# Performance work log

Hardware: AMD Instinct MI355X
Metric: run time of the kernel (lower is better)

Reference implementation:

```python
import jax, jax.numpy as jnp
import numpy as np

IMAGE = 800.0
HIGH_THRESH = 0.7   # torchvision RPN fg_iou_thresh
LOW_THRESH = 0.3    # torchvision RPN bg_iou_thresh
BELOW_LOW = -1      # Matcher.BELOW_LOW_THRESHOLD
BETWEEN = -2        # Matcher.BETWEEN_THRESHOLDS


def _make_boxes(key, shape, max_wh):
    # shape = (..., 4) target; build valid xyxy boxes inside the image
    k1, k2 = jax.random.split(key)
    xy = jax.random.uniform(k1, shape[:-1] + (2,)) * (IMAGE - max_wh)
    wh = jax.random.uniform(k2, shape[:-1] + (2,)) * (max_wh - 4.0) + 4.0
    return jnp.concatenate([xy, xy + wh], axis=-1)


def setup_inputs() -> dict:
    key = jax.random.key(0)
    kA, kG, kS, kC = jax.random.split(key, 4)
    B, A, G = 4, 160000, 64
    anchors = _make_boxes(kA, (B, A, 4), 128.0)
    gt_boxes = _make_boxes(kG, (B, G, 4), 200.0)
    # soft score labels in {0, 0.5, 1} style: mostly 1, some <1 (ignored), some 0
    u = jax.random.uniform(kS, (B, G))
    score_labels = jnp.where(u < 0.15, 0.0, jnp.where(u < 0.3, 0.5, 1.0)).astype(jnp.float32)
    confidence_labels = jax.random.randint(kC, (B, G), 0, 2).astype(jnp.int32)
    return {"anchors": anchors, "gt_boxes": gt_boxes,
            "score_labels": score_labels, "confidence_labels": confidence_labels}


def _box_iou(a, b):
    # a: [G,4] gt, b: [A,4] anchors -> [G,A]
    area_a = (a[:, 2] - a[:, 0]) * (a[:, 3] - a[:, 1])          # [G]
    area_b = (b[:, 2] - b[:, 0]) * (b[:, 3] - b[:, 1])          # [A]
    lt = jnp.maximum(a[:, None, :2], b[None, :, :2])            # [G,A,2]
    rb = jnp.minimum(a[:, None, 2:], b[None, :, 2:])            # [G,A,2]
    wh = jnp.clip(rb - lt, 0.0)
    inter = wh[..., 0] * wh[..., 1]                              # [G,A]
    return inter / (area_a[:, None] + area_b[None, :] - inter)


def _matcher(mq):
    # torchvision Matcher with allow_low_quality_matches=True. mq: [G,A]
    matched_vals = mq.max(axis=0)                                # [A]
    matches = mq.argmax(axis=0).astype(jnp.int32)                # [A]
    m = jnp.where(matched_vals < LOW_THRESH, BELOW_LOW,
                  jnp.where(matched_vals < HIGH_THRESH, BETWEEN, matches))
    # restore, for each gt, anchors achieving that gt's max IoU
    highest_per_gt = mq.max(axis=1, keepdims=True)               # [G,1]
    low_quality = (mq == highest_per_gt).any(axis=0)             # [A]
    return jnp.where(low_quality, matches, m)


def _assign_one(anchors, gt, scores, confs):
    mq = _box_iou(gt, anchors)                                   # [G,A]
    midx = _matcher(mq)                                          # [A]
    cl = jnp.clip(midx, 0)
    matched_gt = gt[cl]                                          # [A,4]
    pos = midx >= 0
    labels = pos.astype(jnp.float32)
    labels = jnp.minimum(labels, scores[cl])
    labels = jnp.where(midx == BELOW_LOW, 0.0, labels)
    labels = jnp.where(midx == BETWEEN, -1.0, labels)
    labels = jnp.where((scores[cl] < 1.0) & pos, -1.0, labels)
    labels = jnp.where((confs[cl] == 0) & pos, -1.0, labels)
    return labels, matched_gt


def reference(anchors, gt_boxes, score_labels, confidence_labels):
    labels, matched_gt_boxes = jax.vmap(_assign_one)(anchors, gt_boxes, score_labels, confidence_labels)
    return labels, matched_gt_boxes
```

## Files before the change

kernel.cpp:

```cpp
#include <hip/hip_runtime.h>

constexpr int NB = 4;
constexpr int NA = 160000;
constexpr int NG = 64;

constexpr int P1  = 250;
constexpr int APB = NA / P1;
constexpr int APW = APB / 4;

__device__ __forceinline__ float box_area(float x0, float y0, float x1, float y1) {
#pragma clang fp contract(off)
    return (x1 - x0) * (y1 - y0);
}

__device__ __forceinline__ void inter_denom(float gx0, float gy0, float gx1, float gy1, float garea,
                                            float ax0, float ay0, float ax1, float ay1, float aarea,
                                            float& inter, float& denom) {
#pragma clang fp contract(off)
    float ltx = fmaxf(gx0, ax0);
    float lty = fmaxf(gy0, ay0);
    float rbx = fminf(gx1, ax1);
    float rby = fminf(gy1, ay1);
    float w = fmaxf(rbx - ltx, 0.0f);
    float h = fmaxf(rby - lty, 0.0f);
    inter = w * h;
    float s = garea + aarea;
    denom = s - inter;
}

__device__ __forceinline__ bool frac_gt(float i1, float d1, float i2, float d2) {
#pragma clang fp contract(off)
    float p1 = i1 * d2;
    float p2 = i2 * d1;
    float e1 = fmaf(i1, d2, -p1);
    float e2 = fmaf(i2, d1, -p2);
    return (p1 > p2) || ((p1 == p2) && (e1 > e2));
}

__device__ __forceinline__ float div_rn(float n, float d) {
    float y = __builtin_amdgcn_rcpf(d);
    float e = fmaf(-d, y, 1.0f);
    y = fmaf(e, y, y);
    float q = n * y;
    float r = fmaf(-d, q, n);
    q = fmaf(r, y, q);
    float r2 = fmaf(-d, q, n);
    return fmaf(r2, y, q);
}

__global__ __launch_bounds__(256) void k_part(
        const float* __restrict__ anchors, const float* __restrict__ gts,
        float2* __restrict__ part ) {
    const int b = blockIdx.y;
    const int j = blockIdx.x;
    const int lane = threadIdx.x & 63;
    const int wid = __builtin_amdgcn_readfirstlane(threadIdx.x >> 6);

    const float4* __restrict__ anc =
        reinterpret_cast<const float4*>(anchors) + (size_t)b * NA;
    float4 g = reinterpret_cast<const float4*>(gts)[b * NG + lane];
    float garea = box_area(g.x, g.y, g.z, g.w);

    const int base = j * APB + wid * APW;
    float bi = 0.0f, bd = 1.0f;
#pragma unroll 8
    for (int i = 0; i < APW; ++i) {
        float4 a = anc[base + i];
        float aarea = box_area(a.x, a.y, a.z, a.w);
        float inter, denom;
        inter_denom(g.x, g.y, g.z, g.w, garea, a.x, a.y, a.z, a.w, aarea,
                    inter, denom);
        if (frac_gt(inter, denom, bi, bd)) { bi = inter; bd = denom; }
    }

    __shared__ float pi[4][NG], pd[4][NG];
    pi[wid][lane] = bi;
    pd[wid][lane] = bd;
    __syncthreads();
    if (threadIdx.x < NG) {
        float ci = pi[0][threadIdx.x], cd = pd[0][threadIdx.x];
#pragma unroll
        for (int wv = 1; wv < 4; ++wv) {
            float ni = pi[wv][threadIdx.x], nd = pd[wv][threadIdx.x];
            if (frac_gt(ni, nd, ci, cd)) { ci = ni; cd = nd; }
        }
        part[((size_t)b * P1 + j) * NG + threadIdx.x] = make_float2(ci, cd);
    }
}

__global__ __launch_bounds__(256) void k_assign2(
        const float* __restrict__ anchors, const float* __restrict__ gts,
        const float* __restrict__ scores, const int* __restrict__ confs,
        const float2* __restrict__ part,
        float* __restrict__ labels_out, float4* __restrict__ boxes_out) {
    __shared__ float4 sg[NG];
    __shared__ float2 sah[NG];
    __shared__ float  ssc[NG];
    __shared__ int    scf[NG];
    __shared__ float  rpi[4][NG], rpd[4][NG];

    const int b = blockIdx.y;
    if (threadIdx.x < NG) {
        const int gi = threadIdx.x;
        sg[gi]  = reinterpret_cast<const float4*>(gts)[b * NG + gi];
        ssc[gi] = scores[b * NG + gi];
        scf[gi] = confs[b * NG + gi];
    }

    {
        const int gi = threadIdx.x & 63;
        const int c  = threadIdx.x >> 6;
        float ci = 0.0f, cd = 1.0f;
        for (int p = c; p < P1; p += 4) {
            float2 v = part[((size_t)b * P1 + p) * NG + gi];
            if (frac_gt(v.x, v.y, ci, cd)) { ci = v.x; cd = v.y; }
        }
        rpi[c][gi] = ci;
        rpd[c][gi] = cd;
    }
    __syncthreads();
    if (threadIdx.x < NG) {
        const int gi = threadIdx.x;
        float ci = rpi[0][gi], cd = rpd[0][gi];
#pragma unroll
        for (int wv = 1; wv < 4; ++wv) {
            float ni = rpi[wv][gi], nd = rpd[wv][gi];
            if (frac_gt(ni, nd, ci, cd)) { ci = ni; cd = nd; }
        }
        float4 gv = sg[gi];
        sah[gi] = make_float2(box_area(gv.x, gv.y, gv.z, gv.w),
                              div_rn(ci, cd));
    }
    __syncthreads();

    const int ai = blockIdx.x * 256 + threadIdx.x;
    const float4* __restrict__ anc =
        reinterpret_cast<const float4*>(anchors) + (size_t)b * NA;
    float4 av = anc[ai];
    float aarea = box_area(av.x, av.y, av.z, av.w);

    float best = -1.0f;
    int   matches = 0;
    bool  lowq = false;
#pragma unroll 4
    for (int g = 0; g < NG; ++g) {
        float4 gb = sg[g];
        float2 ah = sah[g];
        float inter, denom;
        inter_denom(gb.x, gb.y, gb.z, gb.w, ah.x,
                    av.x, av.y, av.z, av.w, aarea, inter, denom);
        float v = div_rn(inter, denom);
        if (v > best) { best = v; matches = g; }
        lowq |= (v == ah.y);
    }

    int m    = (best < 0.3f) ? -1 : ((best < 0.7f) ? -2 : matches);
    int midx = lowq ? matches : m;
    int cl   = (midx < 0) ? 0 : midx;

    float4 mg = sg[cl];
    float  sc = ssc[cl];
    int    cf = scf[cl];

    bool pos = (midx >= 0);
    float lab = pos ? 1.0f : 0.0f;
    lab = fminf(lab, sc);
    if (midx == -1) lab = 0.0f;
    if (midx == -2) lab = -1.0f;
    if (sc < 1.0f && pos) lab = -1.0f;
    if (cf == 0 && pos) lab = -1.0f;

    labels_out[(size_t)b * NA + ai] = lab;
    boxes_out[(size_t)b * NA + ai] = mg;
}

__global__ __launch_bounds__(256) void k_gt_highest_fb(
        const float* __restrict__ anchors, const float* __restrict__ gts,
        float* __restrict__ highest ) {
    const int b = blockIdx.y;
    const int lane = threadIdx.x & 63;
    const int wid = __builtin_amdgcn_readfirstlane(threadIdx.x >> 6);

    const float4* __restrict__ anc =
        reinterpret_cast<const float4*>(anchors) + (size_t)b * NA;
    float4 g = reinterpret_cast<const float4*>(gts)[b * NG + lane];
    float garea = box_area(g.x, g.y, g.z, g.w);

    const int base = blockIdx.x * 160 + wid * 40;
    float bi = 0.0f, bd = 1.0f;
#pragma unroll 8
    for (int i = 0; i < 40; ++i) {
        float4 a = anc[base + i];
        float aarea = box_area(a.x, a.y, a.z, a.w);
        float inter, denom;
        inter_denom(g.x, g.y, g.z, g.w, garea, a.x, a.y, a.z, a.w, aarea,
                    inter, denom);
        if (frac_gt(inter, denom, bi, bd)) { bi = inter; bd = denom; }
    }

    __shared__ float pi[4][NG], pd[4][NG];
    pi[wid][lane] = bi;
    pd[wid][lane] = bd;
    __syncthreads();
    if (threadIdx.x < NG) {
        float ci = pi[0][threadIdx.x], cd = pd[0][threadIdx.x];
#pragma unroll
        for (int wv = 1; wv < 4; ++wv) {
            float ni = pi[wv][threadIdx.x], nd = pd[wv][threadIdx.x];
            if (frac_gt(ni, nd, ci, cd)) { ci = ni; cd = nd; }
        }
        atomicMax(reinterpret_cast<int*>(&highest[b * NG + threadIdx.x]),
                  __float_as_int(div_rn(ci, cd)));
    }
}

__global__ __launch_bounds__(256) void k_assign_fb(
        const float* __restrict__ anchors, const float* __restrict__ gts,
        const float* __restrict__ scores, const int* __restrict__ confs,
        const float* __restrict__ highest,
        float* __restrict__ labels_out, float4* __restrict__ boxes_out) {
    __shared__ float4 sg[NG];
    __shared__ float2 sah[NG];
    __shared__ float  ssc[NG];
    __shared__ int    scf[NG];

    const int b = blockIdx.y;
    if (threadIdx.x < NG) {
        const int gi = threadIdx.x;
        float4 gv = reinterpret_cast<const float4*>(gts)[b * NG + gi];
        sg[gi] = gv;
        sah[gi] = make_float2(box_area(gv.x, gv.y, gv.z, gv.w),
                              highest[b * NG + gi]);
        ssc[gi] = scores[b * NG + gi];
        scf[gi] = confs[b * NG + gi];
    }
    __syncthreads();

    const int ai = blockIdx.x * 256 + threadIdx.x;
    const float4* __restrict__ anc =
        reinterpret_cast<const float4*>(anchors) + (size_t)b * NA;
    float4 av = anc[ai];
    float aarea = box_area(av.x, av.y, av.z, av.w);

    float best = -1.0f;
    int   matches = 0;
    bool  lowq = false;
#pragma unroll 4
    for (int g = 0; g < NG; ++g) {
        float4 gb = sg[g];
        float2 ah = sah[g];
        float inter, denom;
        inter_denom(gb.x, gb.y, gb.z, gb.w, ah.x,
                    av.x, av.y, av.z, av.w, aarea, inter, denom);
        float v = div_rn(inter, denom);
        if (v > best) { best = v; matches = g; }
        lowq |= (v == ah.y);
    }

    int m    = (best < 0.3f) ? -1 : ((best < 0.7f) ? -2 : matches);
    int midx = lowq ? matches : m;
    int cl   = (midx < 0) ? 0 : midx;

    float4 mg = sg[cl];
    float  sc = ssc[cl];
    int    cf = scf[cl];

    bool pos = (midx >= 0);
    float lab = pos ? 1.0f : 0.0f;
    lab = fminf(lab, sc);
    if (midx == -1) lab = 0.0f;
    if (midx == -2) lab = -1.0f;
    if (sc < 1.0f && pos) lab = -1.0f;
    if (cf == 0 && pos) lab = -1.0f;

    labels_out[(size_t)b * NA + ai] = lab;
    boxes_out[(size_t)b * NA + ai] = mg;
}

extern "C" void kernel_launch(void* const* d_in, const int* in_sizes, int n_in,
                              void* d_out, int out_size, void* d_ws, size_t ws_size,
                              hipStream_t stream) {
    const float* anchors = (const float*)d_in[0];
    const float* gts     = (const float*)d_in[1];
    const float* scores  = (const float*)d_in[2];
    const int*   confs   = (const int*)d_in[3];

    float* labels_out = (float*)d_out;
    float4* boxes_out = (float4*)((float*)d_out + (size_t)NB * NA);

    const size_t need = (size_t)NB * P1 * NG * sizeof(float2);
    if (ws_size >= need) {
        float2* part = (float2*)d_ws;
        dim3 g1(P1, NB), g2(625, NB), blk(256);
        k_part<<<g1, blk, 0, stream>>>(anchors, gts, part);
        k_assign2<<<g2, blk, 0, stream>>>(anchors, gts, scores, confs, part,
                                          labels_out, boxes_out);
    } else {
        float* highest = (float*)d_ws;
        hipMemsetAsync(d_ws, 0, (size_t)NB * NG * sizeof(float), stream);
        dim3 g1(1000, NB), g2(625, NB), blk(256);
        k_gt_highest_fb<<<g1, blk, 0, stream>>>(anchors, gts, highest);
        k_assign_fb<<<g2, blk, 0, stream>>>(anchors, gts, scores, confs, highest,
                                            labels_out, boxes_out);
    }
}
```

Before: 156.1 us.

## Process four anchors per thread in assign and widen partial-max blocks

The assign kernel now handles 1024 anchors per block, four per thread, so each shared-memory GT load is reused across four anchors. Each block therefore repeats the cross-partition reduction of partial maxima only once per 1024 anchors instead of once per 256. The partial-max kernel moves to 1024-thread blocks with 16 waves of 40 anchors each, keeping 250 partitions. This adds register pressure and leaves fewer blocks in the assign grid, which could lower occupancy.

```diff
diff --git a/kernel.cpp b/kernel.cpp
--- a/kernel.cpp
+++ b/kernel.cpp
@@ -4,9 +4,11 @@
 constexpr int NA = 160000;
 constexpr int NG = 64;
 
-constexpr int P1  = 250;
-constexpr int APB = NA / P1;
-constexpr int APW = APB / 4;
+constexpr int P1   = 250;
+constexpr int APB1 = NA / P1;
+constexpr int APW  = 40;
+constexpr int AB2  = 1024;
+constexpr int GX2  = (NA + AB2 - 1) / AB2;
 
 __device__ __forceinline__ float box_area(float x0, float y0, float x1, float y1) {
 #pragma clang fp contract(off)
@@ -48,7 +50,7 @@
     return fmaf(r2, y, q);
 }
 
-__global__ __launch_bounds__(256) void k_part(
+__global__ __launch_bounds__(1024) void k_part(
         const float* __restrict__ anchors, const float* __restrict__ gts,
         float2* __restrict__ part ) {
     const int b = blockIdx.y;
@@ -61,7 +63,7 @@
     float4 g = reinterpret_cast<const float4*>(gts)[b * NG + lane];
     float garea = box_area(g.x, g.y, g.z, g.w);
 
-    const int base = j * APB + wid * APW;
+    const int base = j * APB1 + wid * APW;
     float bi = 0.0f, bd = 1.0f;
 #pragma unroll 8
     for (int i = 0; i < APW; ++i) {
@@ -73,14 +75,14 @@
         if (frac_gt(inter, denom, bi, bd)) { bi = inter; bd = denom; }
     }
 
-    __shared__ float pi[4][NG], pd[4][NG];
+    __shared__ float pi[16][NG], pd[16][NG];
     pi[wid][lane] = bi;
     pd[wid][lane] = bd;
     __syncthreads();
     if (threadIdx.x < NG) {
         float ci = pi[0][threadIdx.x], cd = pd[0][threadIdx.x];
 #pragma unroll
-        for (int wv = 1; wv < 4; ++wv) {
+        for (int wv = 1; wv < 16; ++wv) {
             float ni = pi[wv][threadIdx.x], nd = pd[wv][threadIdx.x];
             if (frac_gt(ni, nd, ci, cd)) { ci = ni; cd = nd; }
         }
@@ -111,6 +113,7 @@
         const int gi = threadIdx.x & 63;
         const int c  = threadIdx.x >> 6;
         float ci = 0.0f, cd = 1.0f;
+#pragma unroll 4
         for (int p = c; p < P1; p += 4) {
             float2 v = part[((size_t)b * P1 + p) * NG + gi];
             if (frac_gt(v.x, v.y, ci, cd)) { ci = v.x; cd = v.y; }
@@ -130,6 +133,127 @@
         float4 gv = sg[gi];
         sah[gi] = make_float2(box_area(gv.x, gv.y, gv.z, gv.w),
                               div_rn(ci, cd));
+    }
+    __syncthreads();
+
+    const int base2 = blockIdx.x * AB2;
+    const float4* __restrict__ anc =
+        reinterpret_cast<const float4*>(anchors) + (size_t)b * NA;
+
+    float4 av[4];
+    float  aarea[4];
+    float  best[4]    = {-1.0f, -1.0f, -1.0f, -1.0f};
+    int    matches[4] = {0, 0, 0, 0};
+    bool   lowq[4]    = {false, false, false, false};
+#pragma unroll
+    for (int k = 0; k < 4; ++k) {
+        int ai = base2 + threadIdx.x + k * 256;
+        int ac = ai < NA ? ai : NA - 1;
+        av[k] = anc[ac];
+        aarea[k] = box_area(av[k].x, av[k].y, av[k].z, av[k].w);
+    }
+
+#pragma unroll 2
+    for (int g = 0; g < NG; ++g) {
+        float4 gb = sg[g];
+        float2 ah = sah[g];
+#pragma unroll
+        for (int k = 0; k < 4; ++k) {
+            float inter, denom;
+            inter_denom(gb.x, gb.y, gb.z, gb.w, ah.x,
+                        av[k].x, av[k].y, av[k].z, av[k].w, aarea[k],
+                        inter, denom);
+            float v = div_rn(inter, denom);
+            if (v > best[k]) { best[k] = v; matches[k] = g; }
+            lowq[k] |= (v == ah.y);
+        }
+    }
+
+#pragma unroll
+    for (int k = 0; k < 4; ++k) {
+        int ai = base2 + threadIdx.x + k * 256;
+        if (ai >= NA) continue;
+
+        int m    = (best[k] < 0.3f) ? -1 : ((best[k] < 0.7f) ? -2 : matches[k]);
+        int midx = lowq[k] ? matches[k] : m;
+        int cl   = (midx < 0) ? 0 : midx;
+
+        float4 mg = sg[cl];
+        float  sc = ssc[cl];
+        int    cf = scf[cl];
+
+        bool pos = (midx >= 0);
+        float lab = pos ? 1.0f : 0.0f;
+        lab = fminf(lab, sc);
+        if (midx == -1) lab = 0.0f;
+        if (midx == -2) lab = -1.0f;
+        if (sc < 1.0f && pos) lab = -1.0f;
+        if (cf == 0 && pos) lab = -1.0f;
+
+        labels_out[(size_t)b * NA + ai] = lab;
+        boxes_out[(size_t)b * NA + ai] = mg;
+    }
+}
+
+__global__ __launch_bounds__(256) void k_gt_highest_fb(
+        const float* __restrict__ anchors, const float* __restrict__ gts,
+        float* __restrict__ highest ) {
+    const int b = blockIdx.y;
+    const int lane = threadIdx.x & 63;
+    const int wid = __builtin_amdgcn_readfirstlane(threadIdx.x >> 6);
+
+    const float4* __restrict__ anc =
+        reinterpret_cast<const float4*>(anchors) + (size_t)b * NA;
+    float4 g = reinterpret_cast<const float4*>(gts)[b * NG + lane];
+    float garea = box_area(g.x, g.y, g.z, g.w);
+
+    const int base = blockIdx.x * 160 + wid * 40;
+    float bi = 0.0f, bd = 1.0f;
+#pragma unroll 8
+    for (int i = 0; i < 40; ++i) {
+        float4 a = anc[base + i];
+        float aarea = box_area(a.x, a.y, a.z, a.w);
+        float inter, denom;
+        inter_denom(g.x, g.y, g.z, g.w, garea, a.x, a.y, a.z, a.w, aarea,
+                    inter, denom);
+        if (frac_gt(inter, denom, bi, bd)) { bi = inter; bd = denom; }
+    }
+
+    __shared__ float pi[4][NG], pd[4][NG];
+    pi[wid][lane] = bi;
+    pd[wid][lane] = bd;
+    __syncthreads();
+    if (threadIdx.x < NG) {
+        float ci = pi[0][threadIdx.x], cd = pd[0][threadIdx.x];
+#pragma unroll
+        for (int wv = 1; wv < 4; ++wv) {
+            float ni = pi[wv][threadIdx.x], nd = pd[wv][threadIdx.x];
+            if (frac_gt(ni, nd, ci, cd)) { ci = ni; cd = nd; }
+        }
+        atomicMax(reinterpret_cast<int*>(&highest[b * NG + threadIdx.x]),
+                  __float_as_int(div_rn(ci, cd)));
+    }
+}
+
+__global__ __launch_bounds__(256) void k_assign_fb(
+        const float* __restrict__ anchors, const float* __restrict__ gts,
+        const float* __restrict__ scores, const int* __restrict__ confs,
+        const float* __restrict__ highest,
+        float* __restrict__ labels_out, float4* __restrict__ boxes_out) {
+    __shared__ float4 sg[NG];
+    __shared__ float2 sah[NG];
+    __shared__ float  ssc[NG];
+    __shared__ int    scf[NG];
+
+    const int b = blockIdx.y;
+    if (threadIdx.x < NG) {
+        const int gi = threadIdx.x;
+        float4 gv = reinterpret_cast<const float4*>(gts)[b * NG + gi];
+        sg[gi] = gv;
+        sah[gi] = make_float2(box_area(gv.x, gv.y, gv.z, gv.w),
+                              highest[b * NG + gi]);
+        ssc[gi] = scores[b * NG + gi];
+        scf[gi] = confs[b * NG + gi];
     }
     __syncthreads();
 
@@ -174,109 +298,6 @@
     boxes_out[(size_t)b * NA + ai] = mg;
 }
 
-__global__ __launch_bounds__(256) void k_gt_highest_fb(
-        const float* __restrict__ anchors, const float* __restrict__ gts,
-        float* __restrict__ highest ) {
-    const int b = blockIdx.y;
-    const int lane = threadIdx.x & 63;
-    const int wid = __builtin_amdgcn_readfirstlane(threadIdx.x >> 6);
-
-    const float4* __restrict__ anc =
-        reinterpret_cast<const float4*>(anchors) + (size_t)b * NA;
-    float4 g = reinterpret_cast<const float4*>(gts)[b * NG + lane];
-    float garea = box_area(g.x, g.y, g.z, g.w);
-
-    const int base = blockIdx.x * 160 + wid * 40;
-    float bi = 0.0f, bd = 1.0f;
-#pragma unroll 8
-    for (int i = 0; i < 40; ++i) {
-        float4 a = anc[base + i];
-        float aarea = box_area(a.x, a.y, a.z, a.w);
-        float inter, denom;
-        inter_denom(g.x, g.y, g.z, g.w, garea, a.x, a.y, a.z, a.w, aarea,
-                    inter, denom);
-        if (frac_gt(inter, denom, bi, bd)) { bi = inter; bd = denom; }
-    }
-
-    __shared__ float pi[4][NG], pd[4][NG];
-    pi[wid][lane] = bi;
-    pd[wid][lane] = bd;
-    __syncthreads();
-    if (threadIdx.x < NG) {
-        float ci = pi[0][threadIdx.x], cd = pd[0][threadIdx.x];
-#pragma unroll
-        for (int wv = 1; wv < 4; ++wv) {
-            float ni = pi[wv][threadIdx.x], nd = pd[wv][threadIdx.x];
-            if (frac_gt(ni, nd, ci, cd)) { ci = ni; cd = nd; }
-        }
-        atomicMax(reinterpret_cast<int*>(&highest[b * NG + threadIdx.x]),
-                  __float_as_int(div_rn(ci, cd)));
-    }
-}
-
-__global__ __launch_bounds__(256) void k_assign_fb(
-        const float* __restrict__ anchors, const float* __restrict__ gts,
-        const float* __restrict__ scores, const int* __restrict__ confs,
-        const float* __restrict__ highest,
-        float* __restrict__ labels_out, float4* __restrict__ boxes_out) {
-    __shared__ float4 sg[NG];
-    __shared__ float2 sah[NG];
-    __shared__ float  ssc[NG];
-    __shared__ int    scf[NG];
-
-    const int b = blockIdx.y;
-    if (threadIdx.x < NG) {
-        const int gi = threadIdx.x;
-        float4 gv = reinterpret_cast<const float4*>(gts)[b * NG + gi];
-        sg[gi] = gv;
-        sah[gi] = make_float2(box_area(gv.x, gv.y, gv.z, gv.w),
-                              highest[b * NG + gi]);
-        ssc[gi] = scores[b * NG + gi];
-        scf[gi] = confs[b * NG + gi];
-    }
-    __syncthreads();
-
-    const int ai = blockIdx.x * 256 + threadIdx.x;
-    const float4* __restrict__ anc =
-        reinterpret_cast<const float4*>(anchors) + (size_t)b * NA;
-    float4 av = anc[ai];
-    float aarea = box_area(av.x, av.y, av.z, av.w);
-
-    float best = -1.0f;
-    int   matches = 0;
-    bool  lowq = false;
-#pragma unroll 4
-    for (int g = 0; g < NG; ++g) {
-        float4 gb = sg[g];
-        float2 ah = sah[g];
-        float inter, denom;
-        inter_denom(gb.x, gb.y, gb.z, gb.w, ah.x,
-                    av.x, av.y, av.z, av.w, aarea, inter, denom);
-        float v = div_rn(inter, denom);
-        if (v > best) { best = v; matches = g; }
-        lowq |= (v == ah.y);
-    }
-
-    int m    = (best < 0.3f) ? -1 : ((best < 0.7f) ? -2 : matches);
-    int midx = lowq ? matches : m;
-    int cl   = (midx < 0) ? 0 : midx;
-
-    float4 mg = sg[cl];
-    float  sc = ssc[cl];
-    int    cf = scf[cl];
-
-    bool pos = (midx >= 0);
-    float lab = pos ? 1.0f : 0.0f;
-    lab = fminf(lab, sc);
-    if (midx == -1) lab = 0.0f;
-    if (midx == -2) lab = -1.0f;
-    if (sc < 1.0f && pos) lab = -1.0f;
-    if (cf == 0 && pos) lab = -1.0f;
-
-    labels_out[(size_t)b * NA + ai] = lab;
-    boxes_out[(size_t)b * NA + ai] = mg;
-}
-
 extern "C" void kernel_launch(void* const* d_in, const int* in_sizes, int n_in,
                               void* d_out, int out_size, void* d_ws, size_t ws_size,
                               hipStream_t stream) {
@@ -291,16 +312,16 @@
     const size_t need = (size_t)NB * P1 * NG * sizeof(float2);
     if (ws_size >= need) {
         float2* part = (float2*)d_ws;
-        dim3 g1(P1, NB), g2(625, NB), blk(256);
-        k_part<<<g1, blk, 0, stream>>>(anchors, gts, part);
-        k_assign2<<<g2, blk, 0, stream>>>(anchors, gts, scores, confs, part,
-                                          labels_out, boxes_out);
+        dim3 g1(P1, NB), g2(GX2, NB);
+        k_part<<<g1, dim3(1024), 0, stream>>>(anchors, gts, part);
+        k_assign2<<<g2, dim3(256), 0, stream>>>(anchors, gts, scores, confs,
+                                                part, labels_out, boxes_out);
     } else {
         float* highest = (float*)d_ws;
         hipMemsetAsync(d_ws, 0, (size_t)NB * NG * sizeof(float), stream);
         dim3 g1(1000, NB), g2(625, NB), blk(256);
         k_gt_highest_fb<<<g1, blk, 0, stream>>>(anchors, gts, highest);
-        k_assign_fb<<<g2, blk, 0, stream>>>(anchors, gts, scores, confs, highest,
-                                            labels_out, boxes_out);
-    }
-}
+        k_assign_fb<<<g2, blk, 0, stream>>>(anchors, gts, scores, confs,
+                                            highest, labels_out, boxes_out);
+    }
+}
```

Result: faster. 144.2 us (-7.6%).
